# Optimization experiments

Hardware: AMD Instinct MI355X
Metric: run time of the kernel (lower is better)

## Reference

```python
import jax, jax.numpy as jnp
import numpy as np

D_MODEL = 1024
N_HEADS = 16
HEAD_DIM = D_MODEL // N_HEADS
FF_DIM = 1024  # repo bug: linear2 is Linear(d_model, ff_dim); ff_dim==d_model required for residual
EPS = 1e-5


def _linear_params(k, d_in, d_out):
    kw, kb = jax.random.split(k)
    bound = 1.0 / np.sqrt(d_in)
    W = jax.random.uniform(kw, (d_out, d_in), minval=-bound, maxval=bound, dtype=jnp.float32)
    b = jax.random.uniform(kb, (d_out,), minval=-bound, maxval=bound, dtype=jnp.float32)
    return W, b


def setup_inputs() -> dict:
    key = jax.random.key(0)
    ks = jax.random.split(key, 8)
    src = jax.random.normal(ks[0], (4, 2048, D_MODEL), dtype=jnp.float32)
    Wq, bq = _linear_params(ks[1], D_MODEL, D_MODEL)
    Wk, bk = _linear_params(ks[2], D_MODEL, D_MODEL)
    Wv, bv = _linear_params(ks[3], D_MODEL, D_MODEL)
    Wo, bo = _linear_params(ks[4], D_MODEL, D_MODEL)
    W1, b1 = _linear_params(ks[5], D_MODEL, FF_DIM)
    W2, b2 = _linear_params(ks[6], D_MODEL, FF_DIM)
    g1 = jnp.ones((D_MODEL,), jnp.float32); be1 = jnp.zeros((D_MODEL,), jnp.float32)
    g2 = jnp.ones((D_MODEL,), jnp.float32); be2 = jnp.zeros((D_MODEL,), jnp.float32)
    return {"src": src, "Wq": Wq, "bq": bq, "Wk": Wk, "bk": bk, "Wv": Wv, "bv": bv,
            "Wo": Wo, "bo": bo, "W1": W1, "b1": b1, "W2": W2, "b2": b2,
            "g1": g1, "be1": be1, "g2": g2, "be2": be2}


def _layernorm(x, g, b):
    mu = jnp.mean(x, axis=-1, keepdims=True)
    var = jnp.var(x, axis=-1, keepdims=True)
    return (x - mu) * jax.lax.rsqrt(var + EPS) * g + b


def _mha(x, Wq, bq, Wk, bk, Wv, bv, Wo, bo):
    B, S, _ = x.shape
    def proj(W, b):
        return (x @ W.T + b).reshape(B, S, N_HEADS, HEAD_DIM).transpose(0, 2, 1, 3)
    Q, K, V = proj(Wq, bq), proj(Wk, bk), proj(Wv, bv)
    scale = jnp.float32(np.sqrt(HEAD_DIM))
    energy = jnp.einsum('bhqd,bhkd->bhqk', Q, K) / scale
    attn = jax.nn.softmax(energy, axis=-1)
    out = jnp.einsum('bhqk,bhkd->bhqd', attn, V)
    out = out.transpose(0, 2, 1, 3).reshape(B, S, D_MODEL)
    return out @ Wo.T + bo


def reference(src, Wq, bq, Wk, bk, Wv, bv, Wo, bo, W1, b1, W2, b2, g1, be1, g2, be2):
    x = src
    x = x + _mha(_layernorm(x, g1, be1), Wq, bq, Wk, bk, Wv, bv, Wo, bo)
    h = _layernorm(x, g2, be2)
    ff = jax.nn.relu(h @ W1.T + b1) @ W2.T + b2
    return x + ff
```

## Files before the change

kernel.cpp:

```cpp
#include <hip/hip_runtime.h>
#include <stdint.h>

typedef __attribute__((ext_vector_type(8))) short    bf16x8;
typedef __attribute__((ext_vector_type(4))) short    bf16x4;
typedef __attribute__((ext_vector_type(4))) float    f32x4;
typedef __attribute__((ext_vector_type(8))) uint16_t u16x8;
typedef __attribute__((ext_vector_type(4))) uint16_t u16x4;

#define D_MODEL 1024
#define SEQ     2048
#define NB      4
#define NH      16
#define HD      64
#define MTOK    8192

__device__ __forceinline__ float bf2f(uint16_t u) {
    union { uint32_t i; float f; } x; x.i = ((uint32_t)u) << 16; return x.f;
}
__device__ __forceinline__ uint16_t f2bf(float f) {
    union { float f; uint32_t i; } x; x.f = f;
    uint32_t r = (x.i + 0x7fffu + ((x.i >> 16) & 1u)) >> 16;
    return (uint16_t)r;
}
__device__ __forceinline__ void gload16(const void* g, void* l) {
    __builtin_amdgcn_global_load_lds(
        (const __attribute__((address_space(1))) unsigned int*)g,
        (__attribute__((address_space(3))) unsigned int*)l, 16, 0, 0);
}
__device__ __forceinline__ bf16x8 lds_ld8(const uint16_t* p) {
    bf16x4 a = *(const bf16x4*)p;
    bf16x4 b = *(const bf16x4*)(p + 4);
    bf16x8 r;
    r[0] = a[0]; r[1] = a[1]; r[2] = a[2]; r[3] = a[3];
    r[4] = b[0]; r[5] = b[1]; r[6] = b[2]; r[7] = b[3];
    return r;
}
__device__ __forceinline__ uint32_t pk_bf16_trunc(float lo, float hi) {
    return __builtin_amdgcn_perm(__float_as_uint(hi), __float_as_uint(lo), 0x07060302u);
}

__global__ __launch_bounds__(256)
void cvt_all(const float* __restrict__ s0, const float* __restrict__ s1,
             const float* __restrict__ s2, const float* __restrict__ s3,
             const float* __restrict__ s4, const float* __restrict__ s5,
             uint16_t* __restrict__ dQKV, uint16_t* __restrict__ dWo,
             uint16_t* __restrict__ dW1, uint16_t* __restrict__ dW2)
{
    const float* srcs[6] = {s0, s1, s2, s3, s4, s5};
    uint16_t* dsts[6] = {dQKV, dQKV + (size_t)D_MODEL * D_MODEL,
                         dQKV + 2 * (size_t)D_MODEL * D_MODEL, dWo, dW1, dW2};
    const float* in = srcs[blockIdx.y];
    uint16_t* out = dsts[blockIdx.y];
    const int i = (blockIdx.x * 256 + threadIdx.x) * 4;
    float4 v = *(const float4*)(in + i);
    u16x4 o;
    o[0] = f2bf(v.x); o[1] = f2bf(v.y); o[2] = f2bf(v.z); o[3] = f2bf(v.w);
    *(u16x4*)(out + i) = o;
}

__global__ __launch_bounds__(256)
void ln_kernel(const float* __restrict__ x, const float* __restrict__ g,
               const float* __restrict__ be, uint16_t* __restrict__ y)
{
    const int row = blockIdx.x;
    const int tid = threadIdx.x;
    const size_t base = (size_t)row * D_MODEL + tid * 4;
    float4 v = *(const float4*)(x + base);
    float f[4] = {v.x, v.y, v.z, v.w};
    float sum = 0.f, sq = 0.f;
#pragma unroll
    for (int e = 0; e < 4; e++) { sum += f[e]; sq += f[e] * f[e]; }
#pragma unroll
    for (int o = 32; o > 0; o >>= 1) { sum += __shfl_down(sum, o); sq += __shfl_down(sq, o); }
    __shared__ float ps[4], pq[4];
    const int lane = tid & 63, wid = tid >> 6;
    if (lane == 0) { ps[wid] = sum; pq[wid] = sq; }
    __syncthreads();
    const float ts = ps[0] + ps[1] + ps[2] + ps[3];
    const float tq = pq[0] + pq[1] + pq[2] + pq[3];
    const float mean = ts * (1.0f / D_MODEL);
    const float var  = tq * (1.0f / D_MODEL) - mean * mean;
    const float rstd = rsqrtf(var + 1e-5f);
    float4 gv = *(const float4*)(g + tid * 4);
    float4 bv = *(const float4*)(be + tid * 4);
    const float gg[4] = {gv.x, gv.y, gv.z, gv.w};
    const float bb[4] = {bv.x, bv.y, bv.z, bv.w};
    u16x4 outv;
#pragma unroll
    for (int e = 0; e < 4; e++)
        outv[e] = f2bf((f[e] - mean) * rstd * gg[e] + bb[e]);
    *(u16x4*)(y + base) = outv;
}

template<int RESID, int RELU, int OUTF32>
__global__ __launch_bounds__(256, 3)
void gemm_bt128(const uint16_t* __restrict__ A, const uint16_t* __restrict__ W,
                const float* __restrict__ bias, const float* __restrict__ resid,
                void* __restrict__ Cv)
{
    __shared__ uint16_t lA[2][128 * 32];
    __shared__ uint16_t lB[2][128 * 32];
    const int tid  = threadIdx.x;
    const int lane = tid & 63;
    const int quad = lane >> 4;
    const int l16  = lane & 15;
    const int wid  = tid >> 6;
    const int wm   = wid >> 1;
    const int wn   = wid & 1;
    const int m0   = blockIdx.y * 128;
    const int n0   = blockIdx.x * 128;

    f32x4 acc[4][4];
#pragma unroll
    for (int i = 0; i < 4; i++)
#pragma unroll
        for (int j = 0; j < 4; j++) acc[i][j] = (f32x4){0.f, 0.f, 0.f, 0.f};

    const int sr = tid >> 2;
    const int sc = (tid & 3) * 8;
    const uint16_t* gA0 = A + (size_t)(m0 + sr) * D_MODEL + sc;
    const uint16_t* gA1 = gA0 + (size_t)64 * D_MODEL;
    const uint16_t* gW0 = W + (size_t)(n0 + sr) * D_MODEL + sc;
    const uint16_t* gW1 = gW0 + (size_t)64 * D_MODEL;

    #define STAGE_BT(k0, b) do {                      \
        gload16(gA0 + (k0), &lA[b][tid * 8]);         \
        gload16(gA1 + (k0), &lA[b][2048 + tid * 8]);  \
        gload16(gW0 + (k0), &lB[b][tid * 8]);         \
        gload16(gW1 + (k0), &lB[b][2048 + tid * 8]);  \
    } while (0)

    #define COMP_BT(b) do {                                                           \
        bf16x8 fa[4], fb[4];                                                          \
        _Pragma("unroll")                                                             \
        for (int i = 0; i < 4; i++)                                                   \
            fa[i] = *(const bf16x8*)&lA[b][(wm * 64 + i * 16 + l16) * 32 + quad * 8]; \
        _Pragma("unroll")                                                             \
        for (int j = 0; j < 4; j++)                                                   \
            fb[j] = *(const bf16x8*)&lB[b][(wn * 64 + j * 16 + l16) * 32 + quad * 8]; \
        _Pragma("unroll")                                                             \
        for (int i = 0; i < 4; i++)                                                   \
            _Pragma("unroll")                                                         \
            for (int j = 0; j < 4; j++)                                               \
                acc[i][j] = __builtin_amdgcn_mfma_f32_16x16x32_bf16(fa[i], fb[j], acc[i][j], 0, 0, 0); \
    } while (0)

    STAGE_BT(0, 0);
    __syncthreads();
    for (int k0 = 0; k0 < D_MODEL; k0 += 64) {
        STAGE_BT(k0 + 32, 1);
        COMP_BT(0);
        __syncthreads();
        if (k0 + 64 < D_MODEL) STAGE_BT(k0 + 64, 0);
        COMP_BT(1);
        __syncthreads();
    }
    #undef STAGE_BT
    #undef COMP_BT

#pragma unroll
    for (int j = 0; j < 4; j++) {
        const int col = n0 + wn * 64 + j * 16 + l16;
        const float bvv = bias[col];
#pragma unroll
        for (int i = 0; i < 4; i++) {
            const int row = m0 + wm * 64 + i * 16 + quad * 4;
#pragma unroll
            for (int r = 0; r < 4; r++) {
                float v = acc[i][j][r] + bvv;
                const size_t idx = (size_t)(row + r) * D_MODEL + col;
                if (RESID) v += resid[idx];
                if (RELU)  v = fmaxf(v, 0.0f);
                if (OUTF32) ((float*)Cv)[idx] = v;
                else        ((uint16_t*)Cv)[idx] = f2bf(v);
            }
        }
    }
}

#define QSCALE 0.18033688f
__global__ __launch_bounds__(256, 3)
void gemm_qkv(const uint16_t* __restrict__ A, const uint16_t* __restrict__ Wqkv,
              const float* __restrict__ bq, const float* __restrict__ bk,
              const float* __restrict__ bv, uint16_t* __restrict__ Qb,
              uint16_t* __restrict__ Kb, uint16_t* __restrict__ Vt)
{
    __shared__ uint16_t lA[2][128 * 32];
    __shared__ uint16_t lB[2][128 * 32];
    const int tid  = threadIdx.x;
    const int lane = tid & 63;
    const int quad = lane >> 4;
    const int l16  = lane & 15;
    const int wid  = tid >> 6;
    const int wm   = wid >> 1;
    const int wn   = wid & 1;
    const int t0   = blockIdx.y * 128;
    const int n0   = blockIdx.x * 128;
    const int which = n0 >> 10;
    const int lc0   = n0 & 1023;

    f32x4 acc[4][4];
#pragma unroll
    for (int i = 0; i < 4; i++)
#pragma unroll
        for (int j = 0; j < 4; j++) acc[i][j] = (f32x4){0.f, 0.f, 0.f, 0.f};

    const int sr = tid >> 2;
    const int sc = (tid & 3) * 8;
    const uint16_t* gA0 = A + (size_t)(t0 + sr) * D_MODEL + sc;
    const uint16_t* gA1 = gA0 + (size_t)64 * D_MODEL;
    const uint16_t* gW0 = Wqkv + (size_t)(n0 + sr) * D_MODEL + sc;
    const uint16_t* gW1 = gW0 + (size_t)64 * D_MODEL;

    #define STAGE_QKV(k0, b) do {                     \
        gload16(gA0 + (k0), &lA[b][tid * 8]);         \
        gload16(gA1 + (k0), &lA[b][2048 + tid * 8]);  \
        gload16(gW0 + (k0), &lB[b][tid * 8]);         \
        gload16(gW1 + (k0), &lB[b][2048 + tid * 8]);  \
    } while (0)

    #define COMP_QKV(b) do {                                                              \
        bf16x8 fa[4], fb[4];                                                              \
        if (which != 2) {                                                                 \
            _Pragma("unroll")                                                             \
            for (int i = 0; i < 4; i++)                                                   \
                fa[i] = *(const bf16x8*)&lA[b][(wm * 64 + i * 16 + l16) * 32 + quad * 8]; \
            _Pragma("unroll")                                                             \
            for (int j = 0; j < 4; j++)                                                   \
                fb[j] = *(const bf16x8*)&lB[b][(wn * 64 + j * 16 + l16) * 32 + quad * 8]; \
        } else {                                                                          \
            _Pragma("unroll")                                                             \
            for (int i = 0; i < 4; i++)                                                   \
                fa[i] = *(const bf16x8*)&lB[b][(wm * 64 + i * 16 + l16) * 32 + quad * 8]; \
            _Pragma("unroll")                                                             \
            for (int j = 0; j < 4; j++)                                                   \
                fb[j] = *(const bf16x8*)&lA[b][(wn * 64 + j * 16 + l16) * 32 + quad * 8]; \
        }                                                                                 \
        _Pragma("unroll")                                                                 \
        for (int i = 0; i < 4; i++)                                                       \
            _Pragma("unroll")                                                             \
            for (int j = 0; j < 4; j++)                                                   \
                acc[i][j] = __builtin_amdgcn_mfma_f32_16x16x32_bf16(fa[i], fb[j], acc[i][j], 0, 0, 0); \
    } while (0)

    STAGE_QKV(0, 0);
    __syncthreads();
    for (int k0 = 0; k0 < D_MODEL; k0 += 64) {
        STAGE_QKV(k0 + 32, 1);
        COMP_QKV(0);
        __syncthreads();
        if (k0 + 64 < D_MODEL) STAGE_QKV(k0 + 64, 0);
        COMP_QKV(1);
        __syncthreads();
    }
    #undef STAGE_QKV
    #undef COMP_QKV

    if (which != 2) {
        const float* bias = (which == 0) ? bq : bk;
        uint16_t* C = (which == 0) ? Qb : Kb;
        const float alpha = (which == 0) ? QSCALE : 1.0f;
#pragma unroll
        for (int j = 0; j < 4; j++) {
            const int col = lc0 + wn * 64 + j * 16 + l16;
            const float bvv = bias[col];
#pragma unroll
            for (int i = 0; i < 4; i++) {
                const int row = t0 + wm * 64 + i * 16 + quad * 4;
#pragma unroll
                for (int r = 0; r < 4; r++)
                    C[(size_t)(row + r) * D_MODEL + col] = f2bf((acc[i][j][r] + bvv) * alpha);
            }
        }
    } else {
#pragma unroll
        for (int i = 0; i < 4; i++) {
#pragma unroll
            for (int r = 0; r < 4; r++) {
                const int wrow = lc0 + wm * 64 + i * 16 + quad * 4 + r;
                const float bvv = bv[wrow];
#pragma unroll
                for (int j = 0; j < 4; j++) {
                    const int tok = t0 + wn * 64 + j * 16 + l16;
                    Vt[(size_t)wrow * MTOK + tok] = f2bf(acc[i][j][r] + bvv);
                }
            }
        }
    }
}

#define PST 68
__global__ __launch_bounds__(256, 4)
void attn_kernel(const uint16_t* __restrict__ Q, const uint16_t* __restrict__ K,
                 const uint16_t* __restrict__ Vt, uint16_t* __restrict__ O)
{
    __shared__ uint16_t sQP[128 * PST];
    __shared__ uint16_t sK [64 * PST];
    __shared__ uint16_t sVt[64 * PST];
    __shared__ float    sSt[128];

    const int tid  = threadIdx.x;
    const int lane = tid & 63;
    const int quad = lane >> 4;
    const int l16  = lane & 15;
    const int w    = tid >> 6;

    const int bh = blockIdx.x;
    const int h  = bh & (NH - 1);
    const int b  = bh >> 4;
    const int q0 = blockIdx.y * 128;
    const size_t headoff = (size_t)h * HD;
    const size_t bbase   = (size_t)b * SEQ;

    const int r8 = tid >> 3;
    const int c8 = (tid & 7) * 8;

#pragma unroll
    for (int i = 0; i < 4; i++)
        gload16(Q + (bbase + q0 + i * 32 + r8) * D_MODEL + headoff + c8, &sQP[i * 2048 + tid * 8]);
    __syncthreads();

    bf16x8 qa[2][2];
#pragma unroll
    for (int i = 0; i < 2; i++)
#pragma unroll
        for (int ks = 0; ks < 2; ks++)
            qa[i][ks] = *(const bf16x8*)&sQP[(w * 32 + i * 16 + l16) * 64 + ks * 32 + quad * 8];

    f32x4 oacc[2][4];
#pragma unroll
    for (int i = 0; i < 2; i++)
#pragma unroll
        for (int n = 0; n < 4; n++) oacc[i][n] = (f32x4){0.f, 0.f, 0.f, 0.f};
    float lrun[2] = {0.f, 0.f};

    const uint16_t* gK  = K  + bbase * D_MODEL + headoff;
    const uint16_t* gVt = Vt + headoff * MTOK + bbase;

    for (int kv0 = 0; kv0 < SEQ; kv0 += 64) {
        u16x8 kreg[2], vreg[2];
#pragma unroll
        for (int i = 0; i < 2; i++) {
            const int row = i * 32 + r8;
            kreg[i] = *(const u16x8*)(gK + (size_t)(kv0 + row) * D_MODEL + c8);
            vreg[i] = *(const u16x8*)(gVt + (size_t)row * MTOK + kv0 + c8);
        }
        __syncthreads();
#pragma unroll
        for (int i = 0; i < 2; i++) {
            const int row = i * 32 + r8;
            *(u16x4*)&sK [(size_t)row * PST + c8]     = (u16x4){kreg[i][0], kreg[i][1], kreg[i][2], kreg[i][3]};
            *(u16x4*)&sK [(size_t)row * PST + c8 + 4] = (u16x4){kreg[i][4], kreg[i][5], kreg[i][6], kreg[i][7]};
            *(u16x4*)&sVt[(size_t)row * PST + c8]     = (u16x4){vreg[i][0], vreg[i][1], vreg[i][2], vreg[i][3]};
            *(u16x4*)&sVt[(size_t)row * PST + c8 + 4] = (u16x4){vreg[i][4], vreg[i][5], vreg[i][6], vreg[i][7]};
        }
        __syncthreads();

        f32x4 st[4][2];
#pragma unroll
        for (int j = 0; j < 4; j++)
#pragma unroll
            for (int i = 0; i < 2; i++) st[j][i] = (f32x4){0.f, 0.f, 0.f, 0.f};
#pragma unroll
        for (int ks = 0; ks < 2; ks++)
#pragma unroll
            for (int j = 0; j < 4; j++) {
                bf16x8 kb = lds_ld8(&sK[(j * 16 + l16) * PST + ks * 32 + quad * 8]);
#pragma unroll
                for (int i = 0; i < 2; i++)
                    st[j][i] = __builtin_amdgcn_mfma_f32_16x16x32_bf16(kb, qa[i][ks], st[j][i], 0, 0, 0);
            }

#pragma unroll
        for (int i = 0; i < 2; i++) {
            float rs = 0.f;
#pragma unroll
            for (int j = 0; j < 4; j++) {
#pragma unroll
                for (int r = 0; r < 4; r++) {
                    const float p = __builtin_amdgcn_exp2f(st[j][i][r]);
                    st[j][i][r] = p;
                    rs += p;
                }
            }
            lrun[i] += rs;
#pragma unroll
            for (int j = 0; j < 4; j++) {
                uint2 pk;
                pk.x = pk_bf16_trunc(st[j][i][0], st[j][i][1]);
                pk.y = pk_bf16_trunc(st[j][i][2], st[j][i][3]);
                *(uint2*)&sQP[(size_t)(w * 32 + i * 16 + l16) * PST + j * 16 + quad * 4] = pk;
            }
        }

#pragma unroll
        for (int i = 0; i < 2; i++)
#pragma unroll
            for (int ks = 0; ks < 2; ks++) {
                bf16x8 pa = lds_ld8(&sQP[(size_t)(w * 32 + i * 16 + l16) * PST + ks * 32 + quad * 8]);
#pragma unroll
                for (int n = 0; n < 4; n++) {
                    bf16x8 vb = lds_ld8(&sVt[(n * 16 + l16) * PST + ks * 32 + quad * 8]);
                    oacc[i][n] = __builtin_amdgcn_mfma_f32_16x16x32_bf16(pa, vb, oacc[i][n], 0, 0, 0);
                }
            }
    }

#pragma unroll
    for (int i = 0; i < 2; i++) {
        lrun[i] += __shfl_xor(lrun[i], 16);
        lrun[i] += __shfl_xor(lrun[i], 32);
        sSt[w * 32 + i * 16 + l16] = 1.0f / lrun[i];
    }
#pragma unroll
    for (int i = 0; i < 2; i++)
#pragma unroll
        for (int r = 0; r < 4; r++) {
            const size_t row = bbase + q0 + w * 32 + i * 16 + quad * 4 + r;
            const float inv = sSt[w * 32 + i * 16 + quad * 4 + r];
#pragma unroll
            for (int n = 0; n < 4; n++)
                O[row * D_MODEL + headoff + n * 16 + l16] = f2bf(oacc[i][n][r] * inv);
        }
}

extern "C" void kernel_launch(void* const* d_in, const int* in_sizes, int n_in,
                              void* d_out, int out_size, void* d_ws, size_t ws_size,
                              hipStream_t stream)
{
    const float* src = (const float*)d_in[0];
    const float* Wq  = (const float*)d_in[1];
    const float* bq  = (const float*)d_in[2];
    const float* Wk  = (const float*)d_in[3];
    const float* bk  = (const float*)d_in[4];
    const float* Wv  = (const float*)d_in[5];
    const float* bv  = (const float*)d_in[6];
    const float* Wo  = (const float*)d_in[7];
    const float* bo  = (const float*)d_in[8];
    const float* W1  = (const float*)d_in[9];
    const float* b1  = (const float*)d_in[10];
    const float* W2  = (const float*)d_in[11];
    const float* b2  = (const float*)d_in[12];
    const float* g1  = (const float*)d_in[13];
    const float* be1 = (const float*)d_in[14];
    const float* g2  = (const float*)d_in[15];
    const float* be2 = (const float*)d_in[16];
    float* out = (float*)d_out;

    uint16_t* ws  = (uint16_t*)d_ws;
    const size_t BUF = (size_t)MTOK * D_MODEL;
    const size_t WSZ = (size_t)D_MODEL * D_MODEL;
    uint16_t* xn1  = ws;
    uint16_t* Vtb  = ws + BUF;
    uint16_t* wQKV = ws + 2 * BUF;
    uint16_t* wWo  = wQKV + 3 * WSZ;
    uint16_t* wW1  = wWo + WSZ;
    uint16_t* wW2  = wW1 + WSZ;
    uint16_t* Qb   = (uint16_t*)d_out;
    uint16_t* Kb   = Qb + BUF;
    float*    x2   = (float*)d_out;

    dim3 blk(256);
    cvt_all<<<dim3(1024, 6), 256, 0, stream>>>(Wq, Wk, Wv, Wo, W1, W2, wQKV, wWo, wW1, wW2);
    ln_kernel<<<8192, 256, 0, stream>>>(src, g1, be1, xn1);
    gemm_qkv<<<dim3(24, 64), blk, 0, stream>>>(xn1, wQKV, bq, bk, bv, Qb, Kb, Vtb);
    attn_kernel<<<dim3(64, 16), 256, 0, stream>>>(Qb, Kb, Vtb, xn1);
    gemm_bt128<1, 0, 1><<<dim3(8, 64), blk, 0, stream>>>(xn1, wWo, bo, src, x2);
    ln_kernel<<<8192, 256, 0, stream>>>(x2, g2, be2, xn1);
    gemm_bt128<0, 1, 0><<<dim3(8, 64), blk, 0, stream>>>(xn1, wW1, b1, nullptr, Vtb);
    gemm_bt128<1, 0, 1><<<dim3(8, 64), blk, 0, stream>>>(Vtb, wW2, b2, x2, out);
}
```

Measured before the change: 400.8 us.

## Triple-buffer GEMM k-loop with vmcnt waits and halve M-tile for dense GEMMs

Replaces the double-buffered k-loop in the QKV and dense GEMMs with a three-stage ring of LDS buffers. Explicit s_waitcnt vmcnt counts and raw barriers keep two async global-to-LDS loads in flight while one buffer is computed. The Wo/W1/W2 GEMMs also drop from 128x128 to 64x128 tiles, doubling the grid to 1024 blocks so more of the CUs are busy, with occupancy hint raised to 4. The cost is lower operand reuse per block and more LDS per block for QKV, and the hand-counted vmcnt values must match the exact number of issued loads.

```diff
diff --git a/kernel.cpp b/kernel.cpp
--- a/kernel.cpp
+++ b/kernel.cpp
@@ -38,6 +38,10 @@
 __device__ __forceinline__ uint32_t pk_bf16_trunc(float lo, float hi) {
     return __builtin_amdgcn_perm(__float_as_uint(hi), __float_as_uint(lo), 0x07060302u);
 }
+
+#define VM_WAIT(n) asm volatile("s_waitcnt vmcnt(" #n ")" ::: "memory")
+#define RAW_BAR()  __builtin_amdgcn_s_barrier()
+#define SCHED_FENCE() __builtin_amdgcn_sched_barrier(0)
 
 __global__ __launch_bounds__(256)
 void cvt_all(const float* __restrict__ s0, const float* __restrict__ s1,
@@ -93,13 +97,13 @@
 }
 
 template<int RESID, int RELU, int OUTF32>
-__global__ __launch_bounds__(256, 3)
-void gemm_bt128(const uint16_t* __restrict__ A, const uint16_t* __restrict__ W,
-                const float* __restrict__ bias, const float* __restrict__ resid,
-                void* __restrict__ Cv)
-{
-    __shared__ uint16_t lA[2][128 * 32];
-    __shared__ uint16_t lB[2][128 * 32];
+__global__ __launch_bounds__(256, 4)
+void gemm_bt64(const uint16_t* __restrict__ A, const uint16_t* __restrict__ W,
+               const float* __restrict__ bias, const float* __restrict__ resid,
+               void* __restrict__ Cv)
+{
+    __shared__ uint16_t lA[3][64 * 32];
+    __shared__ uint16_t lB[3][128 * 32];
     const int tid  = threadIdx.x;
     const int lane = tid & 63;
     const int quad = lane >> 4;
@@ -107,64 +111,66 @@
     const int wid  = tid >> 6;
     const int wm   = wid >> 1;
     const int wn   = wid & 1;
-    const int m0   = blockIdx.y * 128;
+    const int m0   = blockIdx.y * 64;
     const int n0   = blockIdx.x * 128;
 
-    f32x4 acc[4][4];
-#pragma unroll
-    for (int i = 0; i < 4; i++)
+    f32x4 acc[2][4];
+#pragma unroll
+    for (int i = 0; i < 2; i++)
 #pragma unroll
         for (int j = 0; j < 4; j++) acc[i][j] = (f32x4){0.f, 0.f, 0.f, 0.f};
 
     const int sr = tid >> 2;
     const int sc = (tid & 3) * 8;
     const uint16_t* gA0 = A + (size_t)(m0 + sr) * D_MODEL + sc;
-    const uint16_t* gA1 = gA0 + (size_t)64 * D_MODEL;
     const uint16_t* gW0 = W + (size_t)(n0 + sr) * D_MODEL + sc;
     const uint16_t* gW1 = gW0 + (size_t)64 * D_MODEL;
 
-    #define STAGE_BT(k0, b) do {                      \
+    #define STG_BT(k0, b) do {                        \
         gload16(gA0 + (k0), &lA[b][tid * 8]);         \
-        gload16(gA1 + (k0), &lA[b][2048 + tid * 8]);  \
         gload16(gW0 + (k0), &lB[b][tid * 8]);         \
         gload16(gW1 + (k0), &lB[b][2048 + tid * 8]);  \
     } while (0)
 
-    #define COMP_BT(b) do {                                                           \
-        bf16x8 fa[4], fb[4];                                                          \
+    #define CMP_BT(b) do {                                                            \
+        bf16x8 af[2], bfr[4];                                                         \
         _Pragma("unroll")                                                             \
-        for (int i = 0; i < 4; i++)                                                   \
-            fa[i] = *(const bf16x8*)&lA[b][(wm * 64 + i * 16 + l16) * 32 + quad * 8]; \
+        for (int i = 0; i < 2; i++)                                                   \
+            af[i] = *(const bf16x8*)&lA[b][(wm * 32 + i * 16 + l16) * 32 + quad * 8]; \
         _Pragma("unroll")                                                             \
         for (int j = 0; j < 4; j++)                                                   \
-            fb[j] = *(const bf16x8*)&lB[b][(wn * 64 + j * 16 + l16) * 32 + quad * 8]; \
+            bfr[j] = *(const bf16x8*)&lB[b][(wn * 64 + j * 16 + l16) * 32 + quad * 8];\
         _Pragma("unroll")                                                             \
-        for (int i = 0; i < 4; i++)                                                   \
+        for (int i = 0; i < 2; i++)                                                   \
             _Pragma("unroll")                                                         \
             for (int j = 0; j < 4; j++)                                               \
-                acc[i][j] = __builtin_amdgcn_mfma_f32_16x16x32_bf16(fa[i], fb[j], acc[i][j], 0, 0, 0); \
+                acc[i][j] = __builtin_amdgcn_mfma_f32_16x16x32_bf16(af[i], bfr[j], acc[i][j], 0, 0, 0); \
     } while (0)
 
-    STAGE_BT(0, 0);
-    __syncthreads();
-    for (int k0 = 0; k0 < D_MODEL; k0 += 64) {
-        STAGE_BT(k0 + 32, 1);
-        COMP_BT(0);
-        __syncthreads();
-        if (k0 + 64 < D_MODEL) STAGE_BT(k0 + 64, 0);
-        COMP_BT(1);
-        __syncthreads();
-    }
-    #undef STAGE_BT
-    #undef COMP_BT
+    STG_BT(0, 0); STG_BT(32, 1); STG_BT(64, 2);
+    for (int i = 0; i < 29; ++i) {
+        VM_WAIT(6);
+        RAW_BAR();
+        SCHED_FENCE();
+        const int p = i % 3;
+        CMP_BT(p);
+        SCHED_FENCE();
+        RAW_BAR();
+        STG_BT((i + 3) * 32, p);
+    }
+    VM_WAIT(6); RAW_BAR(); SCHED_FENCE(); CMP_BT(2); SCHED_FENCE();
+    VM_WAIT(3); RAW_BAR(); SCHED_FENCE(); CMP_BT(0); SCHED_FENCE();
+    VM_WAIT(0); RAW_BAR(); SCHED_FENCE(); CMP_BT(1);
+    #undef STG_BT
+    #undef CMP_BT
 
 #pragma unroll
     for (int j = 0; j < 4; j++) {
         const int col = n0 + wn * 64 + j * 16 + l16;
         const float bvv = bias[col];
 #pragma unroll
-        for (int i = 0; i < 4; i++) {
-            const int row = m0 + wm * 64 + i * 16 + quad * 4;
+        for (int i = 0; i < 2; i++) {
+            const int row = m0 + wm * 32 + i * 16 + quad * 4;
 #pragma unroll
             for (int r = 0; r < 4; r++) {
                 float v = acc[i][j][r] + bvv;
@@ -185,8 +191,8 @@
               const float* __restrict__ bv, uint16_t* __restrict__ Qb,
               uint16_t* __restrict__ Kb, uint16_t* __restrict__ Vt)
 {
-    __shared__ uint16_t lA[2][128 * 32];
-    __shared__ uint16_t lB[2][128 * 32];
+    __shared__ uint16_t lA[3][128 * 32];
+    __shared__ uint16_t lB[3][128 * 32];
     const int tid  = threadIdx.x;
     const int lane = tid & 63;
     const int quad = lane >> 4;
@@ -212,14 +218,14 @@
     const uint16_t* gW0 = Wqkv + (size_t)(n0 + sr) * D_MODEL + sc;
     const uint16_t* gW1 = gW0 + (size_t)64 * D_MODEL;
 
-    #define STAGE_QKV(k0, b) do {                     \
+    #define STG_QKV(k0, b) do {                       \
         gload16(gA0 + (k0), &lA[b][tid * 8]);         \
         gload16(gA1 + (k0), &lA[b][2048 + tid * 8]);  \
         gload16(gW0 + (k0), &lB[b][tid * 8]);         \
         gload16(gW1 + (k0), &lB[b][2048 + tid * 8]);  \
     } while (0)
 
-    #define COMP_QKV(b) do {                                                              \
+    #define CMP_QKV(b) do {                                                               \
         bf16x8 fa[4], fb[4];                                                              \
         if (which != 2) {                                                                 \
             _Pragma("unroll")                                                             \
@@ -243,18 +249,22 @@
                 acc[i][j] = __builtin_amdgcn_mfma_f32_16x16x32_bf16(fa[i], fb[j], acc[i][j], 0, 0, 0); \
     } while (0)
 
-    STAGE_QKV(0, 0);
-    __syncthreads();
-    for (int k0 = 0; k0 < D_MODEL; k0 += 64) {
-        STAGE_QKV(k0 + 32, 1);
-        COMP_QKV(0);
-        __syncthreads();
-        if (k0 + 64 < D_MODEL) STAGE_QKV(k0 + 64, 0);
-        COMP_QKV(1);
-        __syncthreads();
-    }
-    #undef STAGE_QKV
-    #undef COMP_QKV
+    STG_QKV(0, 0); STG_QKV(32, 1); STG_QKV(64, 2);
+    for (int i = 0; i < 29; ++i) {
+        VM_WAIT(8);
+        RAW_BAR();
+        SCHED_FENCE();
+        const int p = i % 3;
+        CMP_QKV(p);
+        SCHED_FENCE();
+        RAW_BAR();
+        STG_QKV((i + 3) * 32, p);
+    }
+    VM_WAIT(8); RAW_BAR(); SCHED_FENCE(); CMP_QKV(2); SCHED_FENCE();
+    VM_WAIT(4); RAW_BAR(); SCHED_FENCE(); CMP_QKV(0); SCHED_FENCE();
+    VM_WAIT(0); RAW_BAR(); SCHED_FENCE(); CMP_QKV(1);
+    #undef STG_QKV
+    #undef CMP_QKV
 
     if (which != 2) {
         const float* bias = (which == 0) ? bq : bk;
@@ -465,8 +475,8 @@
     ln_kernel<<<8192, 256, 0, stream>>>(src, g1, be1, xn1);
     gemm_qkv<<<dim3(24, 64), blk, 0, stream>>>(xn1, wQKV, bq, bk, bv, Qb, Kb, Vtb);
     attn_kernel<<<dim3(64, 16), 256, 0, stream>>>(Qb, Kb, Vtb, xn1);
-    gemm_bt128<1, 0, 1><<<dim3(8, 64), blk, 0, stream>>>(xn1, wWo, bo, src, x2);
+    gemm_bt64<1, 0, 1><<<dim3(8, 128), blk, 0, stream>>>(xn1, wWo, bo, src, x2);
     ln_kernel<<<8192, 256, 0, stream>>>(x2, g2, be2, xn1);
-    gemm_bt128<0, 1, 0><<<dim3(8, 64), blk, 0, stream>>>(xn1, wW1, b1, nullptr, Vtb);
-    gemm_bt128<1, 0, 1><<<dim3(8, 64), blk, 0, stream>>>(Vtb, wW2, b2, x2, out);
-}
+    gemm_bt64<0, 1, 0><<<dim3(8, 128), blk, 0, stream>>>(xn1, wW1, b1, nullptr, Vtb);
+    gemm_bt64<1, 0, 1><<<dim3(8, 128), blk, 0, stream>>>(Vtb, wW2, b2, x2, out);
+}
```

After: 381.0 us. 1.05x faster.
